# Kernel optimization log

Hardware: AMD Instinct MI355X
Metric: run time of the kernel (lower is better)

The kernel has to match this reference:

```python
import jax, jax.numpy as jnp
import numpy as np

K = 1024
D = 64
BETA = 0.25
DECAY = 0.99
EPS = 1e-05


def setup_inputs() -> dict:
    key = jax.random.key(0)
    k1, k2 = jax.random.split(key)
    z = jax.random.normal(k1, (32, D, 64, 64), dtype=jnp.float32)
    # nn.init.uniform_(weight, -1/K, 1/K)
    embedding = jax.random.uniform(k2, (K, D), dtype=jnp.float32, minval=-1.0 / K, maxval=1.0 / K)
    # post-_maybe_init_ema_from_embedding state
    cluster_size = jnp.ones((K,), dtype=jnp.float32)
    embed_avg = embedding.copy()
    return {"z": z, "embedding": embedding, "cluster_size": cluster_size, "embed_avg": embed_avg}


def reference(z, embedding, cluster_size, embed_avg):
    B, C, H, W = z.shape
    z_nhwc = jnp.transpose(z, (0, 2, 3, 1))            # [B,H,W,D]
    flat = z_nhwc.reshape(-1, D)                        # [N,D]

    x2 = jnp.sum(flat * flat, axis=1, keepdims=True)    # [N,1]
    w2 = jnp.sum(embedding * embedding, axis=1)         # [K]
    dist = x2 + w2[None, :] - 2.0 * flat @ embedding.T  # [N,K]
    idx = jnp.argmin(dist, axis=1)                      # [N] int

    z_q = embedding[idx].reshape(z_nhwc.shape)          # gather

    # EMA codebook update (training, update=True)
    counts = jax.ops.segment_sum(jnp.ones_like(idx, dtype=jnp.float32), idx, num_segments=K)
    embed_sum = jax.ops.segment_sum(flat, idx, num_segments=K)  # [K,D]
    new_cluster_size = cluster_size * DECAY + (1.0 - DECAY) * counts
    new_embed_avg = embed_avg * DECAY + (1.0 - DECAY) * embed_sum
    n = jnp.sum(new_cluster_size)
    smoothed = (new_cluster_size + EPS) / (n + K * EPS) * n
    new_embedding = new_embed_avg / smoothed[:, None]

    # commitment loss (z_q detached) + straight-through estimator
    loss = BETA * jnp.mean((z_nhwc - jax.lax.stop_gradient(z_q)) ** 2)
    z_q_ste = z_nhwc + jax.lax.stop_gradient(z_q - z_nhwc)
    z_q_out = jnp.transpose(z_q_ste, (0, 3, 1, 2))      # back to [B,C,H,W]
    return (z_q_out, idx, loss, new_embedding, new_cluster_size, new_embed_avg)
```

## Files before the change

### kernel.cpp

```cpp
#include <hip/hip_runtime.h>
#include <hip/hip_bf16.h>

#define NROWS 131072
#define DDIM  64
#define KCODES 1024
#define HW    4096

#define OFF_ZQ   0ull
#define OFF_IDX  8388608ull
#define OFF_LOSS 8519680ull
#define OFF_EMB  8519681ull
#define OFF_NCS  8585217ull
#define OFF_EAVG 8586241ull

#define SCR_B0    34078724ull
#define SCR_WLO   (SCR_B0 + 131072ull)
#define SCR_W2O   (SCR_B0 + 262144ull)
#define LCAP      20480u

#define FWS_KSCR   16777216ull
#define FWS_ES     16777216ull
#define FWS_CNTF   17039360ull
#define FWS_SX2    17043456ull
#define FWS_SMOOTH 17047552ull
#define FWS_LIST   17301504ull
#define FWS_RMIN   17383424ull
#define FWS_CNTR   17547264ull
#define FWS_TOTAL  17547268ull

#define WSO_KSCR   262144ull
#define WSO_LOSSB  786432ull
#define WSO_SMOOTH 788480ull
#define WSO_CNT    792576ull
#define WSO_ESUM   858112ull

#define GAPTHR 8e-5f

typedef __attribute__((ext_vector_type(8))) short bf16x8;
typedef __attribute__((ext_vector_type(4))) float f32x4;

__device__ __forceinline__ float np_sumsq64(const float* v) {
#pragma clang fp contract(off)
    float r0 = v[0]*v[0], r1 = v[1]*v[1], r2 = v[2]*v[2], r3 = v[3]*v[3];
    float r4 = v[4]*v[4], r5 = v[5]*v[5], r6 = v[6]*v[6], r7 = v[7]*v[7];
    for (int i = 8; i < 64; i += 8) {
        r0 += v[i+0]*v[i+0]; r1 += v[i+1]*v[i+1];
        r2 += v[i+2]*v[i+2]; r3 += v[i+3]*v[i+3];
        r4 += v[i+4]*v[i+4]; r5 += v[i+5]*v[i+5];
        r6 += v[i+6]*v[i+6]; r7 += v[i+7]*v[i+7];
    }
    return ((r0+r1)+(r2+r3))+((r4+r5)+(r6+r7));
}
__device__ __forceinline__ float mul_rn(float a, float b) {
#pragma clang fp contract(off)
    return a * b;
}
__device__ __forceinline__ float add_rn(float a, float b) {
#pragma clang fp contract(off)
    return a + b;
}
__device__ __forceinline__ float sub2_rn(float s, float a) {
#pragma clang fp contract(off)
    return s - 2.0f * a;
}
__device__ __forceinline__ unsigned bf16rne(float v) {
    unsigned b = __float_as_uint(v);
    return (b + 0x7FFFu + ((b >> 16) & 1u)) >> 16;
}
__device__ __forceinline__ float bfu2f(unsigned short u) {
    return __uint_as_float(((unsigned)u) << 16);
}
__device__ __forceinline__ unsigned flipf(float v) {
    unsigned b = __float_as_uint(v);
    return b ^ (0x80000000u | (unsigned)((int)b >> 31));
}
__device__ __forceinline__ float unflip_val(unsigned u) {
    u &= 0xFFFFFC00u;
    unsigned mask = 0x80000000u | (unsigned)((int)(~u) >> 31);
    return __uint_as_float(u ^ mask);
}

__global__ __launch_bounds__(256) void prep_kernel(
        const float* __restrict__ emb, unsigned short* __restrict__ wh,
        unsigned short* __restrict__ wl, float* __restrict__ w2,
        float* __restrict__ embT) {
    __shared__ float tile[64][65];
    const int t = threadIdx.x;
    const int kb = blockIdx.x * 64;
#pragma unroll
    for (int i = 0; i < 16; ++i) {
        const int e = t + i * 256;
        const int kl = e >> 6, d = e & 63;
        const float v = emb[(size_t)(kb + kl) * DDIM + d];
        tile[kl][d] = v;
        const unsigned rh = bf16rne(v);
        const float lv = v - bfu2f((unsigned short)rh);
        wh[(size_t)(kb + kl) * DDIM + d] = (unsigned short)rh;
        wl[(size_t)(kb + kl) * DDIM + d] = (unsigned short)bf16rne(lv);
    }
    __syncthreads();
    if (t < 64) w2[kb + t] = np_sumsq64(&tile[t][0]);
#pragma unroll
    for (int i = 0; i < 16; ++i) {
        const int e = t + i * 256;
        const int d = e >> 6, kl = e & 63;
        embT[(size_t)d * KCODES + kb + kl] = tile[kl][d];
    }
}

#define CBLOAD(S, c)                                                          \
    { const size_t a_ = ((size_t)(((c) * 16 + col) * DDIM + grp * 8));        \
      wh##S##0 = *(const bf16x8*)(wh + a_);                                   \
      wh##S##1 = *(const bf16x8*)(wh + a_ + 32);                              \
      wl##S##0 = *(const bf16x8*)(wl + a_);                                   \
      wl##S##1 = *(const bf16x8*)(wl + a_ + 32); }

#define CBCOMP4(S, c)                                                         \
    { const float4 w2v = *(const float4*)&w2g[(c) * 16 + grp * 4];            \
      const float* w2p = (const float*)&w2v;                                  \
      _Pragma("unroll")                                                       \
      for (int rt = 0; rt < 4; ++rt) {                                        \
        f32x4 aA = {0.f,0.f,0.f,0.f}, aB = {0.f,0.f,0.f,0.f};                 \
        aA = __builtin_amdgcn_mfma_f32_16x16x32_bf16(wh##S##0, fx[rt][0], aA, 0, 0, 0); \
        aA = __builtin_amdgcn_mfma_f32_16x16x32_bf16(wl##S##0, fx[rt][0], aA, 0, 0, 0); \
        aB = __builtin_amdgcn_mfma_f32_16x16x32_bf16(wh##S##1, fx[rt][1], aB, 0, 0, 0); \
        aB = __builtin_amdgcn_mfma_f32_16x16x32_bf16(wl##S##1, fx[rt][1], aB, 0, 0, 0); \
        _Pragma("unroll")                                                     \
        for (int r = 0; r < 4; ++r) {                                         \
          const float val = fmaf(-2.f, aA[r] + aB[r], w2p[r]);                \
          const unsigned u = (flipf(val) & 0xFFFFFC00u) |                     \
                             (unsigned)((c) * 16 + grp * 4 + r);              \
          const unsigned mx = m1[rt] > u ? m1[rt] : u;                        \
          m1[rt] = m1[rt] < u ? m1[rt] : u;                                   \
          m2[rt] = m2[rt] < mx ? m2[rt] : mx;                                 \
        } } }

__global__ __launch_bounds__(512, 4) void score2_kernel(
        const float* __restrict__ z, const float* __restrict__ emb,
        const unsigned short* __restrict__ wh, const unsigned short* __restrict__ wl,
        const float* __restrict__ w2g, float* __restrict__ out,
        unsigned short* __restrict__ xT, unsigned* __restrict__ list,
        unsigned long long* __restrict__ rmin, unsigned* __restrict__ counter) {
    __shared__ __attribute__((aligned(16))) unsigned short sxt[64][512];
    __shared__ unsigned k1s[512];

    const int tid = threadIdx.x;
    const int lane = tid & 63, wid = tid >> 6;
    const int col = lane & 15, grp = lane >> 4;
    const int nb = blockIdx.x * 512;
    const int b = nb >> 12, hb = (nb >> 6) & 63;
    const int w4 = (tid & 15) * 4, h8 = (tid >> 4) & 7, dg = tid >> 7;

    {
#pragma unroll
        for (int j = 0; j < 16; ++j) {
            const int d = dg * 16 + j;
            const float4 v = *(const float4*)&z[((size_t)(b * 64 + d)) * HW + (hb + h8) * 64 + w4];
            ushort4 u;
            u.x = (unsigned short)bf16rne(v.x);
            u.y = (unsigned short)bf16rne(v.y);
            u.z = (unsigned short)bf16rne(v.z);
            u.w = (unsigned short)bf16rne(v.w);
            *(ushort4*)&sxt[d][h8 * 64 + w4] = u;
        }
    }
    __syncthreads();

    bf16x8 fx[4][2];
#pragma unroll
    for (int rt = 0; rt < 4; ++rt)
#pragma unroll
        for (int kh = 0; kh < 2; ++kh) {
            const int row = wid * 64 + rt * 16 + col;
            bf16x8 f;
#pragma unroll
            for (int j = 0; j < 8; ++j)
                f[j] = (short)sxt[kh * 32 + grp * 8 + j][row];
            fx[rt][kh] = f;
            *(bf16x8*)&xT[(size_t)(nb + row) * DDIM + kh * 32 + grp * 8] = f;
        }

    unsigned m1[4] = {~0u, ~0u, ~0u, ~0u}, m2[4] = {~0u, ~0u, ~0u, ~0u};
    bf16x8 whA0, whA1, wlA0, wlA1, whB0, whB1, wlB0, wlB1;

    CBLOAD(A, 0)
    for (int c = 0; c < 64; c += 2) {
        CBLOAD(B, c + 1)
        CBCOMP4(A, c)
        if (c + 2 < 64) CBLOAD(A, c + 2)
        CBCOMP4(B, c + 1)
    }

#pragma unroll
    for (int rt = 0; rt < 4; ++rt) {
        for (int off = 16; off <= 32; off <<= 1) {
            const unsigned o1 = (unsigned)__shfl_xor((int)m1[rt], off, 64);
            const unsigned o2 = (unsigned)__shfl_xor((int)m2[rt], off, 64);
            const unsigned mx = m1[rt] > o1 ? m1[rt] : o1;
            m1[rt] = m1[rt] < o1 ? m1[rt] : o1;
            const unsigned t2 = m2[rt] < o2 ? m2[rt] : o2;
            m2[rt] = t2 < mx ? t2 : mx;
        }
    }

    bool flag[4];
    unsigned long long mrt[4];
    unsigned wavecnt = 0;
#pragma unroll
    for (int rt = 0; rt < 4; ++rt) {
        flag[rt] = (grp == 0) &&
                   ((unflip_val(m2[rt]) - unflip_val(m1[rt])) < GAPTHR);
        mrt[rt] = __ballot(flag[rt]);
        wavecnt += (unsigned)__popcll(mrt[rt]);
    }

    if (grp == 0) {
#pragma unroll
        for (int rt = 0; rt < 4; ++rt) {
            const unsigned k = m1[rt] & 1023u;
            out[OFF_IDX + (size_t)(nb + wid * 64 + rt * 16 + col)] = (float)k;
            k1s[wid * 64 + rt * 16 + col] = k;
        }
    }

    unsigned base = 0;
    if (lane == 0 && wavecnt) base = atomicAdd(counter, wavecnt);
    base = (unsigned)__shfl((int)base, 0, 64);
    unsigned offrt = 0;
#pragma unroll
    for (int rt = 0; rt < 4; ++rt) {
        if (flag[rt]) {
            const unsigned offin =
                (unsigned)__popcll(mrt[rt] & ((lane == 0) ? 0ull : (~0ull >> (64 - lane))));
            const unsigned slot = base + offrt + offin;
            if (slot < LCAP) {
                list[slot] = (unsigned)(nb + wid * 64 + rt * 16 + col);
                rmin[slot] = ~0ull;
            }
        }
        offrt += (unsigned)__popcll(mrt[rt]);
    }

    __syncthreads();
    {
        const int r0 = h8 * 64 + w4;
        const float* e0 = emb + (size_t)k1s[r0 + 0] * DDIM;
        const float* e1 = emb + (size_t)k1s[r0 + 1] * DDIM;
        const float* e2 = emb + (size_t)k1s[r0 + 2] * DDIM;
        const float* e3 = emb + (size_t)k1s[r0 + 3] * DDIM;
#pragma unroll
        for (int j = 0; j < 16; ++j) {
            const int d = dg * 16 + j;
            float4 q;
            q.x = e0[d]; q.y = e1[d]; q.z = e2[d]; q.w = e3[d];
            *(float4*)&out[((size_t)(b * 64 + d)) * HW + (hb + h8) * 64 + w4] = q;
        }
    }
}

__global__ __launch_bounds__(256, 1) void rescanb_kernel(
        const float* __restrict__ z, const float* __restrict__ emb,
        const float* __restrict__ w2, const unsigned* __restrict__ list,
        const unsigned* __restrict__ counter,
        unsigned long long* __restrict__ rmin) {
    const int lane = threadIdx.x & 63;
    const int wid = __builtin_amdgcn_readfirstlane(threadIdx.x >> 6);
    unsigned cnt = __builtin_amdgcn_readfirstlane(*counter);
    if (cnt > LCAP) cnt = LCAP;
    if (cnt == 0) return;
    const unsigned W = ((cnt + 63) >> 6) * 8;

    for (unsigned w = blockIdx.x * 4 + wid; w < W; w += gridDim.x * 4) {
        const unsigned g = w >> 3, p = w & 7;
        const unsigned slot = g * 64 + lane;
        const bool valid = slot < cnt;
        const unsigned n = list[valid ? slot : 0];
        const unsigned hw = n & 4095u, bb = n >> 12;

        float x[64];
#pragma unroll
        for (int d = 0; d < 64; ++d)
            x[d] = z[(size_t)(bb * 64 + d) * (size_t)HW + hw];

        float r[8];
#pragma unroll
        for (int j = 0; j < 8; ++j) r[j] = mul_rn(x[j], x[j]);
#pragma unroll
        for (int i = 8; i < 64; i += 8)
#pragma unroll
            for (int j = 0; j < 8; ++j)
                r[j] = add_rn(r[j], mul_rn(x[i + j], x[i + j]));
        const float x2 = add_rn(add_rn(add_rn(r[0], r[1]), add_rn(r[2], r[3])),
                                add_rn(add_rn(r[4], r[5]), add_rn(r[6], r[7])));

        unsigned long long best = ~0ull;
        const int k0 = (int)p * 128;
        for (int k = k0; k < k0 + 128; k += 2) {
            const float* wa = emb + (size_t)k * DDIM;
            const float* wb = wa + DDIM;
            float aa = 0.f, ab = 0.f;
#pragma unroll
            for (int d = 0; d < 64; ++d) {
                aa = fmaf(x[d], wa[d], aa);
                ab = fmaf(x[d], wb[d], ab);
            }
            const float da = sub2_rn(add_rn(x2, w2[k]),     aa);
            const float db = sub2_rn(add_rn(x2, w2[k + 1]), ab);
            const unsigned long long ua =
                ((unsigned long long)flipf(da) << 10) | (unsigned long long)k;
            const unsigned long long ub =
                ((unsigned long long)flipf(db) << 10) | (unsigned long long)(k + 1);
            best = best < ua ? best : ua;
            best = best < ub ? best : ub;
        }
        if (valid) atomicMin(&rmin[slot], best);
    }
}

__global__ __launch_bounds__(256) void fix_kernel(
        const unsigned* __restrict__ list, const unsigned long long* __restrict__ rmin,
        const unsigned* __restrict__ counter, const float* __restrict__ emb,
        float* __restrict__ out) {
    unsigned cnt = *counter;
    if (cnt > LCAP) cnt = LCAP;
    const int lane = threadIdx.x & 63, ws = threadIdx.x >> 6;
    const unsigned t = blockIdx.x * 4 + ws;
    if (t >= cnt) return;
    const unsigned long long u = rmin[t];
    if (u == ~0ull) return;
    const unsigned k = (unsigned)(u & 1023ull);
    const unsigned n = list[t];
    if (lane == 0) out[OFF_IDX + (size_t)n] = (float)k;
    const unsigned hw = n & 4095u, bb = n >> 12;
    out[((size_t)(bb * 64 + lane)) * HW + hw] = emb[(size_t)k * DDIM + lane];
}

__global__ __launch_bounds__(256) void gather_kernel(
        const float* __restrict__ idxf, const unsigned short* __restrict__ xT,
        float* __restrict__ es, float* __restrict__ cntf, float* __restrict__ sx2a) {
    const int k = blockIdx.x;
    const int lane = threadIdx.x & 63, wid = threadIdx.x >> 6;
    const float fk = (float)k;
    float acc = 0.f, s2 = 0.f;
    unsigned cnt = 0;
    const int wbase = wid * 32768;

    float4 cur = *(const float4*)&idxf[wbase + lane * 4];
    for (int it = 0; it < 128; ++it) {
        float4 nxt;
        if (it + 1 < 128)
            nxt = *(const float4*)&idxf[wbase + (it + 1) * 256 + lane * 4];
        const float* cp = (const float*)&cur;
#pragma unroll
        for (int j = 0; j < 4; ++j) {
            unsigned long long m = __ballot(cp[j] == fk);
            cnt += (unsigned)__popcll(m);
            while (m) {
                const int src = __ffsll(m) - 1;
                m &= m - 1;
                const int n = wbase + it * 256 + src * 4 + j;
                const float xv = bfu2f(xT[(size_t)n * DDIM + lane]);
                acc += xv;
                s2 = fmaf(xv, xv, s2);
            }
        }
        cur = nxt;
    }
#pragma unroll
    for (int off = 32; off > 0; off >>= 1) s2 += __shfl_down(s2, off, 64);
    __shared__ float sacc[4][64];
    __shared__ float ssx2[4];
    __shared__ unsigned scnt[4];
    sacc[wid][lane] = acc;
    if (lane == 0) { ssx2[wid] = s2; scnt[wid] = cnt; }
    __syncthreads();
    if (wid == 0) {
        const float t = sacc[0][lane] + sacc[1][lane] + sacc[2][lane] + sacc[3][lane];
        es[(size_t)k * DDIM + lane] = t;
        if (lane == 0) {
            cntf[k] = (float)(scnt[0] + scnt[1] + scnt[2] + scnt[3]);
            sx2a[k] = ssx2[0] + ssx2[1] + ssx2[2] + ssx2[3];
        }
    }
}

__global__ __launch_bounds__(1024) void fin1_f(
        const float* __restrict__ cs, const float* __restrict__ emb,
        float* __restrict__ out, const float* __restrict__ w2,
        const float* __restrict__ es, const float* __restrict__ cntf,
        const float* __restrict__ sx2a, float* __restrict__ smoothed) {
    const int k = threadIdx.x;
    const float cnt = cntf[k];
    const float w2k = w2[k];
    const float* ek = es + (size_t)k * DDIM;
    const float* wk = emb + (size_t)k * DDIM;
    float dt = 0.f;
#pragma unroll
    for (int d = 0; d < DDIM; ++d) dt = fmaf(ek[d], wk[d], dt);
    const float lp = sx2a[k] - 2.f * dt + cnt * w2k;
    const float ncs = fmaf(0.01f, cnt, 0.99f * cs[k]);

    __shared__ float red[1024];
    red[k] = ncs;
    __syncthreads();
    for (int s = 512; s > 0; s >>= 1) {
        if (k < s) red[k] += red[k + s];
        __syncthreads();
    }
    const float nn = red[0];
    __syncthreads();
    red[k] = lp;
    __syncthreads();
    for (int s = 512; s > 0; s >>= 1) {
        if (k < s) red[k] += red[k + s];
        __syncthreads();
    }
    smoothed[k] = (ncs + 1e-5f) / (nn + 1024.f * 1e-5f) * nn;
    out[OFF_NCS + (size_t)k] = ncs;
    if (k == 0) out[OFF_LOSS] = 0.25f * red[0] / 8388608.f;
}

__global__ __launch_bounds__(256) void fin2_f(
        const float* __restrict__ eavg, float* __restrict__ out,
        const float* __restrict__ es, const float* __restrict__ smoothed) {
    const int e = blockIdx.x * 256 + threadIdx.x;
    const float ea = fmaf(0.01f, es[e], 0.99f * eavg[e]);
    out[OFF_EAVG + (size_t)e] = ea;
    out[OFF_EMB  + (size_t)e] = ea / smoothed[e >> 6];
}


#define CBCOMP(S, c)                                                          \
    { const float4 w2v = *(const float4*)&w2s[(c) * 16 + grp * 4];            \
      const float* w2p = (const float*)&w2v;                                  \
      _Pragma("unroll")                                                       \
      for (int rt = 0; rt < 2; ++rt) {                                        \
        f32x4 aA = {0.f,0.f,0.f,0.f}, aB = {0.f,0.f,0.f,0.f};                 \
        aA = __builtin_amdgcn_mfma_f32_16x16x32_bf16(wh##S##0, fx[rt][0], aA, 0, 0, 0); \
        aA = __builtin_amdgcn_mfma_f32_16x16x32_bf16(wl##S##0, fx[rt][0], aA, 0, 0, 0); \
        aB = __builtin_amdgcn_mfma_f32_16x16x32_bf16(wh##S##1, fx[rt][1], aB, 0, 0, 0); \
        aB = __builtin_amdgcn_mfma_f32_16x16x32_bf16(wl##S##1, fx[rt][1], aB, 0, 0, 0); \
        _Pragma("unroll")                                                     \
        for (int r = 0; r < 4; ++r) {                                         \
          const float val = fmaf(-2.f, aA[r] + aB[r], w2p[r]);                \
          const unsigned u = (flipf(val) & 0xFFFFFC00u) |                     \
                             (unsigned)((c) * 16 + grp * 4 + r);              \
          const unsigned mx = m1[rt] > u ? m1[rt] : u;                        \
          m1[rt] = m1[rt] < u ? m1[rt] : u;                                   \
          m2[rt] = m2[rt] < mx ? m2[rt] : mx;                                 \
        } } }

__global__ __launch_bounds__(512, 4) void score_kernel(
        const float* __restrict__ z,
        const unsigned short* __restrict__ wh, const unsigned short* __restrict__ wl,
        const float* __restrict__ w2, unsigned* __restrict__ kscr) {
    __shared__ __attribute__((aligned(16))) unsigned short sxt[64][260];
    __shared__ float w2s[KCODES];

    const int tid = threadIdx.x;
    const int lane = tid & 63, wid = tid >> 6;
    const int col = lane & 15, grp = lane >> 4;
    const int nb = blockIdx.x * 256;
    const int b = nb >> 12, hb = (nb >> 6) & 63;

    for (int i = tid; i < KCODES; i += 512) w2s[i] = w2[i];
    {
        const int h = lane >> 4, w4 = (lane & 15) * 4;
        const int row = h * 64 + w4;
#pragma unroll
        for (int it = 0; it < 8; ++it) {
            const int d = wid + 8 * it;
            const float4 v = *(const float4*)&z[((size_t)(b * 64 + d)) * HW + (hb + h) * 64 + w4];
            ushort4 u;
            u.x = (unsigned short)bf16rne(v.x);
            u.y = (unsigned short)bf16rne(v.y);
            u.z = (unsigned short)bf16rne(v.z);
            u.w = (unsigned short)bf16rne(v.w);
            *(ushort4*)&sxt[d][row] = u;
        }
    }
    __syncthreads();

    bf16x8 fx[2][2];
#pragma unroll
    for (int rt = 0; rt < 2; ++rt)
#pragma unroll
        for (int kh = 0; kh < 2; ++kh) {
            const int row = wid * 32 + rt * 16 + col;
            bf16x8 f;
#pragma unroll
            for (int j = 0; j < 8; ++j)
                f[j] = (short)sxt[kh * 32 + grp * 8 + j][row];
            fx[rt][kh] = f;
        }

    unsigned m1[2] = {~0u, ~0u}, m2[2] = {~0u, ~0u};
    bf16x8 whA0, whA1, wlA0, wlA1, whB0, whB1, wlB0, wlB1;

    CBLOAD(A, 0)
    for (int c = 0; c < 64; c += 2) {
        CBLOAD(B, c + 1)
        CBCOMP(A, c)
        if (c + 2 < 64) CBLOAD(A, c + 2)
        CBCOMP(B, c + 1)
    }
#pragma unroll
    for (int rt = 0; rt < 2; ++rt) {
        for (int off = 16; off <= 32; off <<= 1) {
            const unsigned o1 = (unsigned)__shfl_xor((int)m1[rt], off, 64);
            const unsigned o2 = (unsigned)__shfl_xor((int)m2[rt], off, 64);
            const unsigned mx = m1[rt] > o1 ? m1[rt] : o1;
            m1[rt] = m1[rt] < o1 ? m1[rt] : o1;
            const unsigned t2 = m2[rt] < o2 ? m2[rt] : o2;
            m2[rt] = t2 < mx ? t2 : mx;
        }
        if (grp == 0) {
            const bool fl = (unflip_val(m2[rt]) - unflip_val(m1[rt])) < GAPTHR;
            kscr[nb + wid * 32 + rt * 16 + col] =
                (m1[rt] & 1023u) | (fl ? 0x80000000u : 0u);
        }
    }
}

__global__ __launch_bounds__(512, 4) void output_kernel(
        const float* __restrict__ z, const float* __restrict__ emb,
        const float* __restrict__ embT, const float* __restrict__ w2,
        float* __restrict__ out, const unsigned* __restrict__ kscr,
        float* __restrict__ esum_p, unsigned* __restrict__ cnt_p,
        float* __restrict__ lossb, int pmask) {
    __shared__ __attribute__((aligned(16))) unsigned short sxt[64][260];
    __shared__ unsigned k1s[256];
    __shared__ float redl[8];

    const int tid = threadIdx.x;
    const int lane = tid & 63, wid = tid >> 6;
    const int nb = blockIdx.x * 256;
    const int b = nb >> 12, hb = (nb >> 6) & 63;

    {
        const int h = lane >> 4, w4 = (lane & 15) * 4;
        const int row = h * 64 + w4;
#pragma unroll
        for (int it = 0; it < 8; ++it) {
            const int d = wid + 8 * it;
            const float4 v = *(const float4*)&z[((size_t)(b * 64 + d)) * HW + (hb + h) * 64 + w4];
            ushort4 u;
            u.x = (unsigned short)bf16rne(v.x);
            u.y = (unsigned short)bf16rne(v.y);
            u.z = (unsigned short)bf16rne(v.z);
            u.w = (unsigned short)bf16rne(v.w);
            *(ushort4*)&sxt[d][row] = u;
        }
    }

    unsigned kf = 0;
    if (lane < 32) kf = kscr[nb + wid * 32 + lane];
    int k1 = (int)(kf & 1023u);
    unsigned long long need = __ballot((lane < 32) && (kf & 0x80000000u));
    while (need) {
        const int src = __ffsll(need) - 1;
        need &= need - 1;
        const int nr = nb + wid * 32 + src;
        const int wq = nr & 63, hq = (nr >> 6) & 63, bq = nr >> 12;
        const float xv = z[(size_t)bq * DDIM * HW + (size_t)lane * HW + hq * 64 + wq];
        const float p = mul_rn(xv, xv);
        float r = 0.f;
        for (int i = 0; i < 8; ++i) {
            const float t = __shfl(p, (i << 3) + (lane & 7), 64);
            r = add_rn(r, t);
        }
        const float s01 = add_rn(r, __shfl_xor(r, 1, 64));
        const float s03 = add_rn(s01, __shfl_xor(s01, 2, 64));
        const float s07 = add_rn(s03, __shfl_xor(s03, 4, 64));
        const float x2s = __shfl(s07, 0, 64);

        float acc[16];
#pragma unroll
        for (int j = 0; j < 16; ++j) acc[j] = 0.f;
        for (int d = 0; d < DDIM; ++d) {
            const float xd = __shfl(xv, d, 64);
            const float* ecol = embT + (size_t)d * KCODES + lane;
#pragma unroll
            for (int j = 0; j < 16; ++j)
                acc[j] = fmaf(ecol[64 * j], xd, acc[j]);
        }
        float bv = 1e30f;
        int bk = KCODES;
#pragma unroll
        for (int j = 0; j < 16; ++j) {
            const int kk = lane + 64 * j;
            const float s  = add_rn(x2s, w2[kk]);
            const float dv = sub2_rn(s, acc[j]);
            if (dv < bv) { bv = dv; bk = kk; }
        }
        for (int off = 32; off > 0; off >>= 1) {
            const float ov = __shfl_xor(bv, off, 64);
            const int   ok = __shfl_xor(bk, off, 64);
            if (ov < bv || (ov == bv && ok < bk)) { bv = ov; bk = ok; }
        }
        if (lane == src) k1 = bk;
    }
    if (lane < 32) k1s[wid * 32 + lane] = (unsigned)k1;
    __syncthreads();

    const int part = blockIdx.x & pmask;
    if (tid < 256) {
        const unsigned myk = k1s[tid];
        out[OFF_IDX + (size_t)(nb + tid)] = (float)myk;
        atomicAdd(&cnt_p[part * KCODES + myk], 1u);
    }

    float ls = 0.f;
    {
        const int h = lane >> 4, w4 = (lane & 15) * 4;
        const int row = h * 64 + w4;
#pragma unroll 2
        for (int it = 0; it < 8; ++it) {
            const int d = wid + 8 * it;
            float4 q;
            float* qp = (float*)&q;
#pragma unroll
            for (int j = 0; j < 4; ++j) {
                const unsigned k = k1s[row + j];
                const float wv = emb[(size_t)k * DDIM + d];
                qp[j] = wv;
                const float diff = bfu2f(sxt[d][row + j]) - wv;
                ls = fmaf(diff, diff, ls);
            }
            *(float4*)&out[((size_t)(b * 64 + d)) * HW + (hb + h) * 64 + w4] = q;
        }
    }
#pragma unroll
    for (int off = 32; off > 0; off >>= 1) ls += __shfl_down(ls, off, 64);
    if (lane == 0) redl[wid] = ls;
    __syncthreads();
    if (tid == 0) {
        float t = 0.f;
#pragma unroll
        for (int i = 0; i < 8; ++i) t += redl[i];
        lossb[blockIdx.x] = t;
    }
    {
        float* ep = esum_p + (size_t)part * 65536;
        for (int r = 0; r < 32; ++r) {
            const int row = wid * 32 + r;
            atomicAdd(&ep[(size_t)k1s[row] * DDIM + lane], bfu2f(sxt[lane][row]));
        }
    }
}

__global__ __launch_bounds__(1024) void finalize1_kernel(
        const float* __restrict__ cs, float* __restrict__ out,
        const unsigned* __restrict__ cnt_p, const float* __restrict__ lossb,
        float* __restrict__ smoothed, int P) {
    const int k = threadIdx.x;
    unsigned c = 0;
    for (int p = 0; p < P; ++p) c += cnt_p[p * KCODES + k];
    const float ncs = fmaf(0.01f, (float)c, 0.99f * cs[k]);

    __shared__ float red[1024];
    red[k] = ncs;
    __syncthreads();
    for (int s = 512; s > 0; s >>= 1) {
        if (k < s) red[k] += red[k + s];
        __syncthreads();
    }
    const float nn = red[0];
    smoothed[k] = (ncs + 1e-5f) / (nn + 1024.f * 1e-5f) * nn;
    out[OFF_NCS + (size_t)k] = ncs;

    __syncthreads();
    red[k] = (k < 512) ? lossb[k] : 0.f;
    __syncthreads();
    for (int s = 512; s > 0; s >>= 1) {
        if (k < s) red[k] += red[k + s];
        __syncthreads();
    }
    if (k == 0) out[OFF_LOSS] = 0.25f * red[0] / 8388608.f;
}

__global__ __launch_bounds__(256) void finalize2_kernel(
        const float* __restrict__ eavg, float* __restrict__ out,
        const float* __restrict__ esum_p, const float* __restrict__ smoothed,
        int P) {
    const int e = blockIdx.x * 256 + threadIdx.x;
    float s = 0.f;
    for (int p = 0; p < P; ++p) s += esum_p[(size_t)p * 65536 + e];
    const float ea = fmaf(0.01f, s, 0.99f * eavg[e]);
    out[OFF_EAVG + (size_t)e] = ea;
    out[OFF_EMB  + (size_t)e] = ea / smoothed[e >> 6];
}


extern "C" void kernel_launch(void* const* d_in, const int* in_sizes, int n_in,
                              void* d_out, int out_size, void* d_ws, size_t ws_size,
                              hipStream_t stream) {
    const float* z    = (const float*)d_in[0];
    const float* emb  = (const float*)d_in[1];
    const float* cs   = (const float*)d_in[2];
    const float* eavg = (const float*)d_in[3];
    float* out = (float*)d_out;

    unsigned short* wh = (unsigned short*)((char*)d_out + SCR_B0);
    unsigned short* wl = (unsigned short*)((char*)d_out + SCR_WLO);
    float*          w2 = (float*)((char*)d_out + SCR_W2O);
    char* ws = (char*)d_ws;

    if (ws_size >= FWS_TOTAL) {
        unsigned short*     xT   = (unsigned short*)ws;
        float*              es   = (float*)(ws + FWS_ES);
        float*              cntf = (float*)(ws + FWS_CNTF);
        float*              sx2a = (float*)(ws + FWS_SX2);
        float*              smoo = (float*)(ws + FWS_SMOOTH);
        unsigned*           list = (unsigned*)(ws + FWS_LIST);
        unsigned long long* rmin = (unsigned long long*)(ws + FWS_RMIN);
        unsigned*           cntr = (unsigned*)(ws + FWS_CNTR);
        float*              embT = (float*)(ws + FWS_KSCR);

        (void)hipMemsetAsync(cntr, 0, 4, stream);
        prep_kernel<<<16, 256, 0, stream>>>(emb, wh, wl, w2, embT);
        score2_kernel<<<NROWS / 512, 512, 0, stream>>>(
            z, emb, wh, wl, w2, out, xT, list, rmin, cntr);
        rescanb_kernel<<<256, 256, 0, stream>>>(z, emb, w2, list, cntr, rmin);
        fix_kernel<<<LCAP / 4, 256, 0, stream>>>(list, rmin, cntr, emb, out);
        gather_kernel<<<KCODES, 256, 0, stream>>>(out + OFF_IDX, xT, es, cntf, sx2a);
        fin1_f<<<1, 1024, 0, stream>>>(cs, emb, out, w2, es, cntf, sx2a, smoo);
        fin2_f<<<256, 256, 0, stream>>>(eavg, out, es, smoo);
    } else {
        int P = 1;
        for (int p = 16; p >= 1; p >>= 1)
            if (ws_size >= WSO_ESUM + (size_t)p * 262144ull) { P = p; break; }

        float*    embT   = (float*)ws;
        unsigned* kscr   = (unsigned*)(ws + WSO_KSCR);
        float*    lossb  = (float*)(ws + WSO_LOSSB);
        float*    smooth = (float*)(ws + WSO_SMOOTH);
        unsigned* cnt_p  = (unsigned*)(ws + WSO_CNT);
        float*    esum_p = (float*)(ws + WSO_ESUM);

        (void)hipMemsetAsync(ws + WSO_CNT, 0, 65536 + (size_t)P * 262144ull, stream);
        prep_kernel<<<16, 256, 0, stream>>>(emb, wh, wl, w2, embT);
        score_kernel<<<NROWS / 256, 512, 0, stream>>>(z, wh, wl, w2, kscr);
        output_kernel<<<NROWS / 256, 512, 0, stream>>>(
            z, emb, embT, w2, out, kscr, esum_p, cnt_p, lossb, P - 1);
        finalize1_kernel<<<1, 1024, 0, stream>>>(cs, out, cnt_p, lossb, smooth, P);
        finalize2_kernel<<<256, 256, 0, stream>>>(eavg, out, esum_p, smooth, P);
    }
}
```

Baseline: 302.6 us.

## Stage codebook tiles in LDS via async global_load_lds double buffering

```diff
diff --git a/kernel.cpp b/kernel.cpp
--- a/kernel.cpp
+++ b/kernel.cpp
@@ -39,6 +39,11 @@
 typedef __attribute__((ext_vector_type(8))) short bf16x8;
 typedef __attribute__((ext_vector_type(4))) float f32x4;
 
+#define GLOAD_LDS16(gp, lp)                                                     \
+    __builtin_amdgcn_global_load_lds(                                           \
+        (const __attribute__((address_space(1))) void*)(gp),                    \
+        (__attribute__((address_space(3))) void*)(lp), 16, 0, 0)
+
 __device__ __forceinline__ float np_sumsq64(const float* v) {
 #pragma clang fp contract(off)
     float r0 = v[0]*v[0], r1 = v[1]*v[1], r2 = v[2]*v[2], r3 = v[3]*v[3];
@@ -115,33 +120,14 @@
       wl##S##0 = *(const bf16x8*)(wl + a_);                                   \
       wl##S##1 = *(const bf16x8*)(wl + a_ + 32); }
 
-#define CBCOMP4(S, c)                                                         \
-    { const float4 w2v = *(const float4*)&w2g[(c) * 16 + grp * 4];            \
-      const float* w2p = (const float*)&w2v;                                  \
-      _Pragma("unroll")                                                       \
-      for (int rt = 0; rt < 4; ++rt) {                                        \
-        f32x4 aA = {0.f,0.f,0.f,0.f}, aB = {0.f,0.f,0.f,0.f};                 \
-        aA = __builtin_amdgcn_mfma_f32_16x16x32_bf16(wh##S##0, fx[rt][0], aA, 0, 0, 0); \
-        aA = __builtin_amdgcn_mfma_f32_16x16x32_bf16(wl##S##0, fx[rt][0], aA, 0, 0, 0); \
-        aB = __builtin_amdgcn_mfma_f32_16x16x32_bf16(wh##S##1, fx[rt][1], aB, 0, 0, 0); \
-        aB = __builtin_amdgcn_mfma_f32_16x16x32_bf16(wl##S##1, fx[rt][1], aB, 0, 0, 0); \
-        _Pragma("unroll")                                                     \
-        for (int r = 0; r < 4; ++r) {                                         \
-          const float val = fmaf(-2.f, aA[r] + aB[r], w2p[r]);                \
-          const unsigned u = (flipf(val) & 0xFFFFFC00u) |                     \
-                             (unsigned)((c) * 16 + grp * 4 + r);              \
-          const unsigned mx = m1[rt] > u ? m1[rt] : u;                        \
-          m1[rt] = m1[rt] < u ? m1[rt] : u;                                   \
-          m2[rt] = m2[rt] < mx ? m2[rt] : mx;                                 \
-        } } }
-
-__global__ __launch_bounds__(512, 4) void score2_kernel(
+__global__ __launch_bounds__(512, 2) void score2_kernel(
         const float* __restrict__ z, const float* __restrict__ emb,
         const unsigned short* __restrict__ wh, const unsigned short* __restrict__ wl,
         const float* __restrict__ w2g, float* __restrict__ out,
         unsigned short* __restrict__ xT, unsigned* __restrict__ list,
         unsigned long long* __restrict__ rmin, unsigned* __restrict__ counter) {
     __shared__ __attribute__((aligned(16))) unsigned short sxt[64][512];
+    __shared__ __attribute__((aligned(16))) unsigned short cb[2][2][4][512];
     __shared__ unsigned k1s[512];
 
     const int tid = threadIdx.x;
@@ -180,15 +166,50 @@
             *(bf16x8*)&xT[(size_t)(nb + row) * DDIM + kh * 32 + grp * 8] = f;
         }
 
+    const int pr = wid >> 2, sW = (wid >> 1) & 1, khW = wid & 1;
+    const unsigned short* gsrc = (pr ? wl : wh) + khW * 32 + grp * 8
+                               + (size_t)(sW * 16 + col) * DDIM;
+
+    GLOAD_LDS16(gsrc, &cb[0][pr][sW * 2 + khW][0]);
+    asm volatile("s_waitcnt vmcnt(0)" ::: "memory");
+    __builtin_amdgcn_s_barrier();
+
     unsigned m1[4] = {~0u, ~0u, ~0u, ~0u}, m2[4] = {~0u, ~0u, ~0u, ~0u};
-    bf16x8 whA0, whA1, wlA0, wlA1, whB0, whB1, wlB0, wlB1;
-
-    CBLOAD(A, 0)
-    for (int c = 0; c < 64; c += 2) {
-        CBLOAD(B, c + 1)
-        CBCOMP4(A, c)
-        if (c + 2 < 64) CBLOAD(A, c + 2)
-        CBCOMP4(B, c + 1)
+
+    for (int rd = 0; rd < 32; ++rd) {
+        const int cur = rd & 1;
+        if (rd < 31)
+            GLOAD_LDS16(gsrc + (size_t)(rd + 1) * 32 * DDIM,
+                        &cb[cur ^ 1][pr][sW * 2 + khW][0]);
+#pragma unroll
+        for (int s = 0; s < 2; ++s) {
+            const bf16x8 vh0 = *(const bf16x8*)&cb[cur][0][s * 2 + 0][lane * 8];
+            const bf16x8 vh1 = *(const bf16x8*)&cb[cur][0][s * 2 + 1][lane * 8];
+            const bf16x8 vl0 = *(const bf16x8*)&cb[cur][1][s * 2 + 0][lane * 8];
+            const bf16x8 vl1 = *(const bf16x8*)&cb[cur][1][s * 2 + 1][lane * 8];
+            const int c = rd * 2 + s;
+            const float4 w2v = *(const float4*)&w2g[c * 16 + grp * 4];
+            const float* w2p = (const float*)&w2v;
+#pragma unroll
+            for (int rt = 0; rt < 4; ++rt) {
+                f32x4 aA = {0.f, 0.f, 0.f, 0.f}, aB = {0.f, 0.f, 0.f, 0.f};
+                aA = __builtin_amdgcn_mfma_f32_16x16x32_bf16(vh0, fx[rt][0], aA, 0, 0, 0);
+                aA = __builtin_amdgcn_mfma_f32_16x16x32_bf16(vl0, fx[rt][0], aA, 0, 0, 0);
+                aB = __builtin_amdgcn_mfma_f32_16x16x32_bf16(vh1, fx[rt][1], aB, 0, 0, 0);
+                aB = __builtin_amdgcn_mfma_f32_16x16x32_bf16(vl1, fx[rt][1], aB, 0, 0, 0);
+#pragma unroll
+                for (int r = 0; r < 4; ++r) {
+                    const float val = fmaf(-2.f, aA[r] + aB[r], w2p[r]);
+                    const unsigned u = (flipf(val) & 0xFFFFFC00u) |
+                                       (unsigned)(c * 16 + grp * 4 + r);
+                    const unsigned mx = m1[rt] > u ? m1[rt] : u;
+                    m1[rt] = m1[rt] < u ? m1[rt] : u;
+                    m2[rt] = m2[rt] < mx ? m2[rt] : mx;
+                }
+            }
+        }
+        asm volatile("s_waitcnt vmcnt(0) lgkmcnt(0)" ::: "memory");
+        __builtin_amdgcn_s_barrier();
     }
 
 #pragma unroll
```

Measured after the change: 298.3 us. Within noise of the previous version (-1.4%).
